# Kernel optimization log

Hardware: AMD Instinct MI355X
Metric: run time of the kernel (lower is better)

The kernel has to match this reference:

```python
import jax, jax.numpy as jnp
import numpy as np

B, L, C, D = 32, 256, 16, 128
WORD_VOCAB, CHR_VOCAB = 50000, 128


def conv1d(x, w, b):
    # x: [N, D, T], w: [D_out, D_in, 3], torch Conv1d (cross-correlation), padding=1
    y = jax.lax.conv_general_dilated(x, w, window_strides=(1,), padding=[(1, 1)],
                                     dimension_numbers=('NCH', 'OIH', 'NCH'))
    return y + b[None, :, None]


def setup_inputs() -> dict:
    key = jax.random.key(0)
    k1, k2, k3, k4, k5, k6, k7, k8 = jax.random.split(key, 8)
    word_vector = jax.random.randint(k1, (B, L), 0, WORD_VOCAB)
    words_in_char = jax.random.randint(k2, (B, L, C), 0, CHR_VOCAB)
    # embedding tables, padding_idx=0 -> row 0 is zeros
    word_table = (jax.random.normal(k3, (WORD_VOCAB, D), jnp.float32) * 0.02).at[0].set(0.0)
    chr_table = (jax.random.normal(k4, (CHR_VOCAB, D), jnp.float32) * 0.02).at[0].set(0.0)
    scale = 1.0 / np.sqrt(D * 3)
    conv_chr_w = jax.random.normal(k5, (D, D, 3), jnp.float32) * scale
    conv_chr_b = jax.random.normal(k6, (D,), jnp.float32) * scale
    conv_word_w = jax.random.normal(k7, (D, D, 3), jnp.float32) * scale
    conv_word_b = jax.random.normal(k8, (D,), jnp.float32) * scale
    return dict(word_vector=word_vector, words_in_char=words_in_char,
                word_table=word_table, chr_table=chr_table,
                conv_chr_w=conv_chr_w, conv_chr_b=conv_chr_b,
                conv_word_w=conv_word_w, conv_word_b=conv_word_b)


def reference(word_vector, words_in_char, word_table, chr_table,
              conv_chr_w, conv_chr_b, conv_word_w, conv_word_b):
    # --- char path (batched version of the per-word Python loop) ---
    chr_emb = chr_table[words_in_char]                       # [B, L, C, D]
    x = chr_emb.reshape(B * L, C, D).transpose(0, 2, 1)      # [B*L, D, C]
    word_conv = conv1d(x, conv_chr_w, conv_chr_b)            # [B*L, D, C]
    char_feats = word_conv.max(axis=2).reshape(B, L, D)      # max over char positions
    # --- word path ---
    word_emb = word_table[word_vector]                       # [B, L, D]
    out = conv1d(word_emb.transpose(0, 2, 1), conv_word_w, conv_word_b)  # [B, D, L]
    # stack both branch outputs into one array: [2, B, D, L]
    return jnp.stack([out, char_feats.transpose(0, 2, 1)])
```

## Files before the change

### kernel.cpp

```cpp
#include <hip/hip_runtime.h>

typedef __attribute__((ext_vector_type(8))) short short8;
typedef __attribute__((ext_vector_type(2))) float float2_t;
typedef __attribute__((ext_vector_type(4))) float float4_t;
typedef __attribute__((ext_vector_type(16))) float float16_t;

#define NB 32
#define NL 256
#define ND 128
#define OUT_PLANE (NB * ND * NL)
#define XS 136
#define BUFSZ (18 * XS)
#define FR_WORD 49152
#define CHRB 98304

__device__ inline unsigned short f2bf(float f) {
    union { float f; unsigned int i; } c;
    c.f = f;
    unsigned int r = c.i + 0x7FFFu + ((c.i >> 16) & 1u);
    return (unsigned short)(r >> 16);
}

__global__ void make_frags(const float* __restrict__ Wc,
                           const float* __restrict__ Ww,
                           const float* __restrict__ chrT,
                           unsigned short* __restrict__ out) {
#pragma unroll
    for (int q = 0; q < 4; ++q) {
        int i = blockIdx.x * 1024 + q * 256 + threadIdx.x;
        unsigned short val;
        if (i < FR_WORD) {
            int j    = i & 7;
            int lane = (i >> 3) & 63;
            int nt   = (i >> 9) & 3;
            int s    = i >> 11;
            int dout = nt * 32 + (lane & 31);
            int kk   = s * 16 + ((lane >> 5) & 1) * 8 + j;
            int t    = kk >> 7;
            int d    = kk & 127;
            val = f2bf(Wc[(dout * 128 + d) * 3 + t]);
        } else if (i < CHRB) {
            int ii = i - FR_WORD;
            int j    = ii & 7;
            int lane = (ii >> 3) & 63;
            int nt   = (ii >> 9) & 7;
            int s    = ii >> 12;
            int dout = nt * 16 + (lane & 15);
            int t    = s >> 2;
            int k    = (s & 3) * 32 + ((lane >> 4) & 3) * 8 + j;
            val = f2bf(Ww[(dout * 128 + k) * 3 + t]);
        } else {
            val = f2bf(chrT[i - CHRB]);
        }
        out[i] = val;
    }
}

__global__ __launch_bounds__(128, 2) void conv_kernel(
    const int* __restrict__ wv, const int* __restrict__ wic,
    const float* __restrict__ wordT,
    const unsigned short* __restrict__ ws,
    const float* __restrict__ biasC, const float* __restrict__ biasW,
    float* __restrict__ out) {
    __shared__ unsigned short X[4][BUFSZ];
    const int tid  = threadIdx.x;
    const int wave = tid >> 6, lane = tid & 63;
    const int bid = blockIdx.x;

    if (bid < 1024) {
        const unsigned short* chrB = ws + CHRB;
        const int w0 = bid * 8;
        const int b = w0 >> 8, l0 = w0 & 255;
        const int n32 = lane & 31;
        const int h   = (lane >> 5) & 1;
        const int r15 = lane & 15;
        const int wsel = (lane >> 4) & 1;

        short8 bfrag[24][2];
#pragma unroll
        for (int s = 0; s < 24; ++s)
#pragma unroll
            for (int p = 0; p < 2; ++p)
                bfrag[s][p] = *(const short8*)(
                    ws + (((s * 4 + wave * 2 + p) * 64 + lane) << 3));
        float bc[2];
#pragma unroll
        for (int p = 0; p < 2; ++p) bc[p] = biasC[wave * 64 + p * 32 + n32];

        for (int p = tid; p < XS; p += 128)
#pragma unroll
            for (int q = 0; q < 4; ++q) { X[q][p] = 0; X[q][17 * XS + p] = 0; }

        const int ra = tid >> 4, sub = tid & 15;

#pragma unroll
        for (int q = 0; q < 2; ++q) {
            int j0 = wic[(w0 + q) * 16 + ra];
            int j1 = wic[(w0 + q) * 16 + ra + 8];
            short8 g0 = *(const short8*)(chrB + j0 * 128 + sub * 8);
            short8 g1 = *(const short8*)(chrB + j1 * 128 + sub * 8);
            *(short8*)&X[q][(ra + 1) * XS + sub * 8] = g0;
            *(short8*)&X[q][(ra + 9) * XS + sub * 8] = g1;
        }
        int iA0 = wic[(w0 + 2) * 16 + ra];
        int iA1 = wic[(w0 + 2) * 16 + ra + 8];
        int iC0 = wic[(w0 + 3) * 16 + ra];
        int iC1 = wic[(w0 + 3) * 16 + ra + 8];
        __syncthreads();

#pragma unroll
        for (int j = 0; j < 8; j += 2) {
            const unsigned short* abuf = X[(j + wsel) & 3];

            short8 g0, g1;
            if (j < 6) {
                g0 = *(const short8*)(chrB + iA0 * 128 + sub * 8);
                g1 = *(const short8*)(chrB + iA1 * 128 + sub * 8);
            }

            float16_t acc[2];
#pragma unroll
            for (int p = 0; p < 2; ++p)
#pragma unroll
                for (int e = 0; e < 16; ++e) acc[p][e] = 0.f;

#pragma unroll
            for (int s = 0; s < 12; ++s) {
                short8 a = *(const short8*)&abuf[(r15 + (s >> 3)) * XS +
                                                 (s & 7) * 16 + h * 8];
#pragma unroll
                for (int p = 0; p < 2; ++p)
                    acc[p] = __builtin_amdgcn_mfma_f32_32x32x16_bf16(
                        a, bfrag[s][p], acc[p], 0, 0, 0);
            }

            short8 h0, h1;
            if (j < 6) {
                *(short8*)&X[(j + 2) & 3][(ra + 1) * XS + sub * 8] = g0;
                *(short8*)&X[(j + 2) & 3][(ra + 9) * XS + sub * 8] = g1;
                h0 = *(const short8*)(chrB + iC0 * 128 + sub * 8);
                h1 = *(const short8*)(chrB + iC1 * 128 + sub * 8);
                if (j < 4) {
                    iA0 = wic[(w0 + j + 4) * 16 + ra];
                    iA1 = wic[(w0 + j + 4) * 16 + ra + 8];
                    iC0 = wic[(w0 + j + 5) * 16 + ra];
                    iC1 = wic[(w0 + j + 5) * 16 + ra + 8];
                }
            }

#pragma unroll
            for (int s = 12; s < 24; ++s) {
                short8 a = *(const short8*)&abuf[(r15 + (s >> 3)) * XS +
                                                 (s & 7) * 16 + h * 8];
#pragma unroll
                for (int p = 0; p < 2; ++p)
                    acc[p] = __builtin_amdgcn_mfma_f32_32x32x16_bf16(
                        a, bfrag[s][p], acc[p], 0, 0, 0);
            }

            if (j < 6) {
                *(short8*)&X[(j + 3) & 3][(ra + 1) * XS + sub * 8] = h0;
                *(short8*)&X[(j + 3) & 3][(ra + 9) * XS + sub * 8] = h1;
            }

#pragma unroll
            for (int p = 0; p < 2; ++p) {
                float v0 = acc[p][0], v1 = acc[p][8];
#pragma unroll
                for (int e = 1; e < 8; ++e) {
                    v0 = fmaxf(v0, acc[p][e]);
                    v1 = fmaxf(v1, acc[p][e + 8]);
                }
                v0 = fmaxf(v0, __shfl_xor(v0, 32, 64));
                v1 = fmaxf(v1, __shfl_xor(v1, 32, 64));
                int dout = wave * 64 + p * 32 + n32;
                if (lane < 32) {
                    float2_t st = {v0 + bc[p], v1 + bc[p]};
                    *(float2_t*)&out[OUT_PLANE + b * (ND * NL) + dout * NL +
                                     l0 + j] = st;
                }
            }
            __syncthreads();
        }
    } else {
        const int wb = bid - 1024;
        const int m = lane & 15, quad = lane >> 4;
        const int b = wb >> 4, l0 = (wb & 15) << 4;
        short8 bfrag[12][4];
#pragma unroll
        for (int s = 0; s < 12; ++s)
#pragma unroll
            for (int p = 0; p < 4; ++p)
                bfrag[s][p] = *(const short8*)(
                    ws + FR_WORD + (((s * 8 + wave * 4 + p) * 64 + lane) << 3));
        float bb[4];
#pragma unroll
        for (int p = 0; p < 4; ++p) bb[p] = biasW[wave * 64 + p * 16 + m];

#pragma unroll
        for (int i0 = 0; i0 < 2; ++i0) {
            int i = tid + i0 * 128;
            if (i < 144) {
                int rr = i >> 3, sg = i & 7;
                int l = l0 + rr - 1;
                int idx = (l >= 0 && l < NL) ? wv[b * NL + l] : 0;
                const float4_t* src =
                    (const float4_t*)(wordT + idx * 128 + sg * 16);
                float4_t f0 = src[0], f1 = src[1], f2 = src[2], f3 = src[3];
                unsigned short t16[16];
                t16[0]=f2bf(f0.x); t16[1]=f2bf(f0.y); t16[2]=f2bf(f0.z); t16[3]=f2bf(f0.w);
                t16[4]=f2bf(f1.x); t16[5]=f2bf(f1.y); t16[6]=f2bf(f1.z); t16[7]=f2bf(f1.w);
                t16[8]=f2bf(f2.x); t16[9]=f2bf(f2.y); t16[10]=f2bf(f2.z); t16[11]=f2bf(f2.w);
                t16[12]=f2bf(f3.x); t16[13]=f2bf(f3.y); t16[14]=f2bf(f3.z); t16[15]=f2bf(f3.w);
                *(short8*)&X[0][rr * XS + sg * 16]     = *(const short8*)&t16[0];
                *(short8*)&X[0][rr * XS + sg * 16 + 8] = *(const short8*)&t16[8];
            }
        }
        __syncthreads();

        float4_t acc[4];
#pragma unroll
        for (int p = 0; p < 4; ++p) acc[p] = (float4_t){0.f, 0.f, 0.f, 0.f};
#pragma unroll
        for (int s = 0; s < 12; ++s) {
            short8 a = *(const short8*)&X[0][(m + (s >> 2)) * XS +
                                            (s & 3) * 32 + quad * 8];
#pragma unroll
            for (int p = 0; p < 4; ++p)
                acc[p] = __builtin_amdgcn_mfma_f32_16x16x32_bf16(
                    a, bfrag[s][p], acc[p], 0, 0, 0);
        }

        float* obase = out + b * (ND * NL) + l0 + quad * 4;
#pragma unroll
        for (int p = 0; p < 4; ++p) {
            int dout = wave * 64 + p * 16 + m;
            float4_t pk;
            pk.x = acc[p].x + bb[p];
            pk.y = acc[p].y + bb[p];
            pk.z = acc[p].z + bb[p];
            pk.w = acc[p].w + bb[p];
            *(float4_t*)&obase[dout * NL] = pk;
        }
    }
}

extern "C" void kernel_launch(void* const* d_in, const int* in_sizes, int n_in,
                              void* d_out, int out_size, void* d_ws,
                              size_t ws_size, hipStream_t stream) {
    const int* word_vector   = (const int*)d_in[0];
    const int* words_in_char = (const int*)d_in[1];
    const float* word_table  = (const float*)d_in[2];
    const float* chr_table   = (const float*)d_in[3];
    const float* conv_chr_w  = (const float*)d_in[4];
    const float* conv_chr_b  = (const float*)d_in[5];
    const float* conv_word_w = (const float*)d_in[6];
    const float* conv_word_b = (const float*)d_in[7];
    float* out            = (float*)d_out;
    unsigned short* wsp   = (unsigned short*)d_ws;

    make_frags<<<112, 256, 0, stream>>>(conv_chr_w, conv_word_w, chr_table, wsp);
    conv_kernel<<<1536, 128, 0, stream>>>(word_vector, words_in_char,
                                          word_table, wsp,
                                          conv_chr_b, conv_word_b, out);
}
```

Before: 104.5 us.

## Stage char-path outputs in LDS for vectorized stores; vectorize fragment prep

The char-path epilogue no longer writes float2 pairs scattered across output rows on every iteration. It accumulates the 8 positions per block in a small shared-memory tile, then each thread writes its output row with two float4 stores. The weight-fragment preparation kernel now has each thread build 8 bf16 values and write them as one 16-byte store, with half the blocks. This costs 4KB of extra LDS per block, which may affect occupancy.

Result: faster. 102.3 us (-2.1%).

```diff
diff --git a/kernel.cpp b/kernel.cpp
--- a/kernel.cpp
+++ b/kernel.cpp
@@ -25,35 +25,38 @@
                            const float* __restrict__ Ww,
                            const float* __restrict__ chrT,
                            unsigned short* __restrict__ out) {
-#pragma unroll
-    for (int q = 0; q < 4; ++q) {
-        int i = blockIdx.x * 1024 + q * 256 + threadIdx.x;
-        unsigned short val;
-        if (i < FR_WORD) {
-            int j    = i & 7;
-            int lane = (i >> 3) & 63;
-            int nt   = (i >> 9) & 3;
-            int s    = i >> 11;
-            int dout = nt * 32 + (lane & 31);
-            int kk   = s * 16 + ((lane >> 5) & 1) * 8 + j;
-            int t    = kk >> 7;
-            int d    = kk & 127;
-            val = f2bf(Wc[(dout * 128 + d) * 3 + t]);
-        } else if (i < CHRB) {
-            int ii = i - FR_WORD;
-            int j    = ii & 7;
-            int lane = (ii >> 3) & 63;
-            int nt   = (ii >> 9) & 7;
-            int s    = ii >> 12;
-            int dout = nt * 16 + (lane & 15);
-            int t    = s >> 2;
-            int k    = (s & 3) * 32 + ((lane >> 4) & 3) * 8 + j;
-            val = f2bf(Ww[(dout * 128 + k) * 3 + t]);
-        } else {
-            val = f2bf(chrT[i - CHRB]);
-        }
-        out[i] = val;
+    const int i0 = (blockIdx.x * 256 + threadIdx.x) * 8;
+    unsigned short v[8];
+    if (i0 < FR_WORD) {
+        int lane = (i0 >> 3) & 63;
+        int nt   = (i0 >> 9) & 3;
+        int s    = i0 >> 11;
+        int dout = nt * 32 + (lane & 31);
+        int kk0  = s * 16 + ((lane >> 5) & 1) * 8;
+        int t    = kk0 >> 7;
+        int d0   = kk0 & 127;
+        const float* src = Wc + (dout * 128 + d0) * 3 + t;
+#pragma unroll
+        for (int j = 0; j < 8; ++j) v[j] = f2bf(src[j * 3]);
+    } else if (i0 < CHRB) {
+        int ii   = i0 - FR_WORD;
+        int lane = (ii >> 3) & 63;
+        int nt   = (ii >> 9) & 7;
+        int s    = ii >> 12;
+        int dout = nt * 16 + (lane & 15);
+        int t    = s >> 2;
+        int k0   = (s & 3) * 32 + ((lane >> 4) & 3) * 8;
+        const float* src = Ww + (dout * 128 + k0) * 3 + t;
+#pragma unroll
+        for (int j = 0; j < 8; ++j) v[j] = f2bf(src[j * 3]);
+    } else {
+        const float* src = chrT + (i0 - CHRB);
+        float4_t f0 = *(const float4_t*)(src);
+        float4_t f1 = *(const float4_t*)(src + 4);
+        v[0] = f2bf(f0.x); v[1] = f2bf(f0.y); v[2] = f2bf(f0.z); v[3] = f2bf(f0.w);
+        v[4] = f2bf(f1.x); v[5] = f2bf(f1.y); v[6] = f2bf(f1.z); v[7] = f2bf(f1.w);
     }
+    *(short8*)&out[i0] = *(const short8*)v;
 }
 
 __global__ __launch_bounds__(128, 2) void conv_kernel(
@@ -63,6 +66,7 @@
     const float* __restrict__ biasC, const float* __restrict__ biasW,
     float* __restrict__ out) {
     __shared__ unsigned short X[4][BUFSZ];
+    __shared__ float OT[8][128];
     const int tid  = threadIdx.x;
     const int wave = tid >> 6, lane = tid & 63;
     const int bid = blockIdx.x;
@@ -173,14 +177,24 @@
                 }
                 v0 = fmaxf(v0, __shfl_xor(v0, 32, 64));
                 v1 = fmaxf(v1, __shfl_xor(v1, 32, 64));
-                int dout = wave * 64 + p * 32 + n32;
                 if (lane < 32) {
-                    float2_t st = {v0 + bc[p], v1 + bc[p]};
-                    *(float2_t*)&out[OUT_PLANE + b * (ND * NL) + dout * NL +
-                                     l0 + j] = st;
+                    int dout = wave * 64 + p * 32 + n32;
+                    OT[j][dout]     = v0 + bc[p];
+                    OT[j + 1][dout] = v1 + bc[p];
                 }
             }
             __syncthreads();
+        }
+
+        {
+            float r[8];
+#pragma unroll
+            for (int e = 0; e < 8; ++e) r[e] = OT[e][tid];
+            float* obase = out + OUT_PLANE + b * (ND * NL) + tid * NL + l0;
+            float4_t s0 = {r[0], r[1], r[2], r[3]};
+            float4_t s1 = {r[4], r[5], r[6], r[7]};
+            *(float4_t*)&obase[0] = s0;
+            *(float4_t*)&obase[4] = s1;
         }
     } else {
         const int wb = bid - 1024;
@@ -259,7 +273,7 @@
     float* out            = (float*)d_out;
     unsigned short* wsp   = (unsigned short*)d_ws;
 
-    make_frags<<<112, 256, 0, stream>>>(conv_chr_w, conv_word_w, chr_table, wsp);
+    make_frags<<<56, 256, 0, stream>>>(conv_chr_w, conv_word_w, chr_table, wsp);
     conv_kernel<<<1536, 128, 0, stream>>>(word_vector, words_in_char,
                                           word_table, wsp,
                                           conv_chr_b, conv_word_b, out);
```
